# Optimization experiments

Measured on AMD Instinct MI355X. Metric: run time of the kernel, lower is better.

## Reference

```python
import jax, jax.numpy as jnp
import numpy as np

D = 448  # state_dim == input_dim == output_dim

def _param(key, shape):
    # matches torch.rand(shape) * 0.1 + 0.001
    return jax.random.uniform(key, shape, dtype=jnp.float32) * 0.1 + 0.001

def setup_inputs() -> dict:
    key = jax.random.key(0)
    ks = jax.random.split(key, 9)
    x = jax.random.normal(ks[0], (8, 4096, D), dtype=jnp.float32)
    return {
        "x": x,
        "W_q": _param(ks[1], (D, D)),
        "W_k": _param(ks[2], (D, D)),
        "W_v": _param(ks[3], (D, D)),
        "W_o": _param(ks[4], (D, D)),
        "SSM_A": _param(ks[5], (D, D)),
        "SSM_B": _param(ks[6], (D, D)),
        "SSM_C": _param(ks[7], (D, D)),
    }

def reference(x, W_q, W_k, W_v, W_o, SSM_A, SSM_B, SSM_C):
    # seq_len=4096 > threshold=256 -> quadratic SSM path.
    # structured_processing's einsum 'bsd,dd->bsd' multiplies elementwise by
    # the diagonal of the matrix; the block loop is redundant, so we apply the
    # diagonal scale over the whole sequence in one fused op.
    q = jnp.einsum('bsi,id->bsd', x, W_q)
    k = jnp.einsum('bsi,id->bsd', x, W_k)
    v = jnp.einsum('bsi,id->bsd', x, W_v)
    ssm = (q * jnp.diagonal(SSM_A)
           + k * jnp.diagonal(SSM_B)
           + v * jnp.diagonal(SSM_C))
    # dropout is identity in eval mode
    return jnp.einsum('bsd,do->bso', ssm, W_o)
```

## Files before the change

kernel.cpp:

```cpp
#include <hip/hip_runtime.h>
#include <hip/hip_bf16.h>

#define DDIM 448
#define NSTEP 14

typedef __hip_bfloat16 bf16;
typedef __attribute__((ext_vector_type(8))) short short8;
typedef __attribute__((ext_vector_type(4))) float f32x4;

__device__ __forceinline__ short bf_bits(float f) {
    bf16 h = __float2bfloat16(f);
    return *reinterpret_cast<short*>(&h);
}

__device__ __forceinline__ void async16(const bf16* g, bf16* l) {
    __builtin_amdgcn_global_load_lds(
        (const __attribute__((address_space(1))) void*)g,
        (__attribute__((address_space(3))) void*)l, 16, 0, 0);
}

__global__ __launch_bounds__(256) void prep_wc(
    const float* __restrict__ Wq, const float* __restrict__ Wk,
    const float* __restrict__ Wv, const float* __restrict__ Wo,
    const float* __restrict__ Ad, const float* __restrict__ Bd,
    const float* __restrict__ Cd, bf16* __restrict__ Wt)
{
    __shared__ __align__(16) bf16 As[64 * 32];
    __shared__ __align__(16) bf16 Bs[64 * 32];
    __shared__ float da[DDIM], db[DDIM], dc[DDIM];

    const int tid  = threadIdx.x;
    const int i0   = blockIdx.x * 64;
    const int o0   = blockIdx.y * 64;
    const int lane = tid & 63;
    const int wid  = tid >> 6;
    const int wm   = wid >> 1, wn = wid & 1;
    const int m_   = lane & 15, kq = lane >> 4;

    for (int d = tid; d < DDIM; d += 256) {
        da[d] = Ad[d * DDIM + d];
        db[d] = Bd[d * DDIM + d];
        dc[d] = Cd[d * DDIM + d];
    }

    const int dr  = tid >> 3;
    const int oc8 = (tid & 7) * 8;
    const int ir  = tid >> 2;
    const int dc8 = (tid & 3) * 8;

    f32x4 acc[2][2] = {};

    f32x4 w0 = *(const f32x4*)(Wo + dr * DDIM + o0 + oc8);
    f32x4 w1 = *(const f32x4*)(Wo + dr * DDIM + o0 + oc8 + 4);
    f32x4 q0 = *(const f32x4*)(Wq + (i0 + ir) * DDIM + dc8);
    f32x4 q1 = *(const f32x4*)(Wq + (i0 + ir) * DDIM + dc8 + 4);
    f32x4 t0 = *(const f32x4*)(Wk + (i0 + ir) * DDIM + dc8);
    f32x4 t1 = *(const f32x4*)(Wk + (i0 + ir) * DDIM + dc8 + 4);
    f32x4 v0 = *(const f32x4*)(Wv + (i0 + ir) * DDIM + dc8);
    f32x4 v1 = *(const f32x4*)(Wv + (i0 + ir) * DDIM + dc8 + 4);

    for (int k0 = 0; k0 < DDIM; k0 += 32) {
        __syncthreads();
        #pragma unroll
        for (int j = 0; j < 4; ++j) {
            As[(oc8 + j) * 32 + dr]     = __float2bfloat16(w0[j]);
            As[(oc8 + 4 + j) * 32 + dr] = __float2bfloat16(w1[j]);
        }
        short8 e;
        #pragma unroll
        for (int j = 0; j < 4; ++j) {
            e[j]     = bf_bits(q0[j] * da[k0 + dc8 + j]
                             + t0[j] * db[k0 + dc8 + j]
                             + v0[j] * dc[k0 + dc8 + j]);
            e[j + 4] = bf_bits(q1[j] * da[k0 + dc8 + 4 + j]
                             + t1[j] * db[k0 + dc8 + 4 + j]
                             + v1[j] * dc[k0 + dc8 + 4 + j]);
        }
        *(short8*)&Bs[ir * 32 + dc8] = e;
        __syncthreads();

        const int kn = (k0 + 32 < DDIM) ? k0 + 32 : 0;
        w0 = *(const f32x4*)(Wo + (kn + dr) * DDIM + o0 + oc8);
        w1 = *(const f32x4*)(Wo + (kn + dr) * DDIM + o0 + oc8 + 4);
        q0 = *(const f32x4*)(Wq + (i0 + ir) * DDIM + kn + dc8);
        q1 = *(const f32x4*)(Wq + (i0 + ir) * DDIM + kn + dc8 + 4);
        t0 = *(const f32x4*)(Wk + (i0 + ir) * DDIM + kn + dc8);
        t1 = *(const f32x4*)(Wk + (i0 + ir) * DDIM + kn + dc8 + 4);
        v0 = *(const f32x4*)(Wv + (i0 + ir) * DDIM + kn + dc8);
        v1 = *(const f32x4*)(Wv + (i0 + ir) * DDIM + kn + dc8 + 4);

        short8 af[2], bfr[2];
        #pragma unroll
        for (int mi = 0; mi < 2; ++mi)
            af[mi] = *(const short8*)&As[(wm * 32 + mi * 16 + m_) * 32 + kq * 8];
        #pragma unroll
        for (int ni = 0; ni < 2; ++ni)
            bfr[ni] = *(const short8*)&Bs[(wn * 32 + ni * 16 + m_) * 32 + kq * 8];
        #pragma unroll
        for (int mi = 0; mi < 2; ++mi)
            #pragma unroll
            for (int ni = 0; ni < 2; ++ni)
                acc[mi][ni] = __builtin_amdgcn_mfma_f32_16x16x32_bf16(
                    af[mi], bfr[ni], acc[mi][ni], 0, 0, 0);
    }

    #pragma unroll
    for (int mi = 0; mi < 2; ++mi)
        #pragma unroll
        for (int ni = 0; ni < 2; ++ni) {
            const int o = o0 + wm * 32 + mi * 16 + kq * 4;
            const int i = i0 + wn * 32 + ni * 16 + m_;
            bf16* dst = Wt + (i >> 5) * (DDIM * 32) + (i & 31);
            #pragma unroll
            for (int r = 0; r < 4; ++r)
                dst[(o + r) * 32] = __float2bfloat16(acc[mi][ni][r]);
        }
}

__global__ __launch_bounds__(512, 2) void gemm_xwc(
    const float* __restrict__ X, const bf16* __restrict__ Wt,
    float* __restrict__ out)
{
    __shared__ __align__(16) char smem[102400];

    const int tid  = threadIdx.x;
    const int lane = tid & 63;
    const int wid  = tid >> 6;
    const int wr   = wid >> 2;
    const int wc   = wid & 3;
    const int m_   = lane & 15;
    const int kq   = lane >> 4;
    const int row0 = blockIdx.x * 128;

    const int ar = tid >> 2;
    const int ac = (tid & 3) * 8;
    const float* agp = X + (row0 + ar) * DDIM + ac;

    const bf16* bgp = Wt + wc * 7 * 512 + lane * 8;

    f32x4 acc[4][7] = {};

    f32x4 a0 = *(const f32x4*)(agp);
    f32x4 a1 = *(const f32x4*)(agp + 4);
    {
        bf16* A0 = (bf16*)smem;
        short8 w;
        #pragma unroll
        for (int j = 0; j < 4; ++j) {
            w[j] = bf_bits(a0[j]); w[j + 4] = bf_bits(a1[j]);
        }
        *(short8*)&A0[ar * 32 + ac] = w;
    }
    a0 = *(const f32x4*)(agp + 32);
    a1 = *(const f32x4*)(agp + 36);
    if (wid < 4) {
        bf16* B0 = (bf16*)(smem + 16384);
        bf16* B1 = (bf16*)(smem + 16384 + 28672);
        #pragma unroll
        for (int j = 0; j < 7; ++j)
            async16(bgp + j * 512, B0 + (wc * 7 + j) * 512);
        const bf16* b1 = bgp + DDIM * 32;
        #pragma unroll
        for (int j = 0; j < 7; ++j)
            async16(b1 + j * 512, B1 + (wc * 7 + j) * 512);
    }
    asm volatile("s_waitcnt vmcnt(7)" ::: "memory");
    asm volatile("s_waitcnt lgkmcnt(0)" ::: "memory");
    __builtin_amdgcn_s_barrier();

    int bcur = 0;
    int bn2  = 2;
    for (int s = 0; s < NSTEP; ++s) {
        const bf16* Ac = (const bf16*)(smem + ((s & 1) << 13));
        const bf16* Bc = (const bf16*)(smem + 16384 + bcur * 28672);

        if (s + 1 < NSTEP) {
            bf16* An = (bf16*)(smem + (((s + 1) & 1) << 13));
            short8 w;
            #pragma unroll
            for (int j = 0; j < 4; ++j) {
                w[j] = bf_bits(a0[j]); w[j + 4] = bf_bits(a1[j]);
            }
            *(short8*)&An[ar * 32 + ac] = w;
        }
        if (s + 2 < NSTEP) {
            const int k2 = (s + 2) * 32;
            a0 = *(const f32x4*)(agp + k2);
            a1 = *(const f32x4*)(agp + k2 + 4);
        }
        if (s + 2 < NSTEP && wid < 4) {
            bf16* Bn = (bf16*)(smem + 16384 + bn2 * 28672);
            const bf16* bsrc = bgp + (s + 2) * (DDIM * 32);
            #pragma unroll
            for (int j = 0; j < 7; ++j)
                async16(bsrc + j * 512, Bn + (wc * 7 + j) * 512);
        }

        short8 af[4], bfr[7];
        #pragma unroll
        for (int mi = 0; mi < 4; ++mi)
            af[mi] = *(const short8*)&Ac[(wr * 64 + mi * 16 + m_) * 32 + kq * 8];
        #pragma unroll
        for (int ni = 0; ni < 7; ++ni)
            bfr[ni] = *(const short8*)&Bc[(wc * 112 + ni * 16 + m_) * 32 + kq * 8];

        #pragma unroll
        for (int mi = 0; mi < 4; ++mi)
            #pragma unroll
            for (int ni = 0; ni < 7; ++ni)
                acc[mi][ni] = __builtin_amdgcn_mfma_f32_16x16x32_bf16(
                    af[mi], bfr[ni], acc[mi][ni], 0, 0, 0);

        if (s < NSTEP - 2) {
            asm volatile("s_waitcnt vmcnt(9)" ::: "memory");
        } else {
            asm volatile("s_waitcnt vmcnt(0)" ::: "memory");
        }
        asm volatile("s_waitcnt lgkmcnt(0)" ::: "memory");
        __builtin_amdgcn_s_barrier();

        bcur = (bcur == 2) ? 0 : bcur + 1;
        bn2  = (bn2  == 2) ? 0 : bn2  + 1;
    }

    float* Cb = (float*)(smem + 16384);
    #pragma unroll
    for (int t = 0; t < 4; ++t) {
        if (wr == (t >> 1)) {
            #pragma unroll
            for (int mi2 = 0; mi2 < 2; ++mi2) {
                const int mi = (t & 1) * 2 + mi2;
                #pragma unroll
                for (int ni = 0; ni < 7; ++ni) {
                    const int col = wc * 112 + ni * 16 + m_;
                    #pragma unroll
                    for (int r = 0; r < 4; ++r)
                        Cb[(mi2 * 16 + kq * 4 + r) * 452 + col] = acc[mi][ni][r];
                }
            }
        }
        __syncthreads();
        const f32x4* Cb4 = (const f32x4*)Cb;
        f32x4* dst4 = (f32x4*)(out + (row0 + t * 32) * DDIM);
        #pragma unroll
        for (int j = 0; j < 7; ++j) {
            const int v   = j * 512 + tid;
            const int row = v / 112;
            const int cw  = v - row * 112;
            dst4[v] = Cb4[row * 113 + cw];
        }
        __syncthreads();
    }
}

extern "C" void kernel_launch(void* const* d_in, const int* in_sizes, int n_in,
                              void* d_out, int out_size, void* d_ws, size_t ws_size,
                              hipStream_t stream) {
    const float* x  = (const float*)d_in[0];
    const float* Wq = (const float*)d_in[1];
    const float* Wk = (const float*)d_in[2];
    const float* Wv = (const float*)d_in[3];
    const float* Wo = (const float*)d_in[4];
    const float* Ad = (const float*)d_in[5];
    const float* Bd = (const float*)d_in[6];
    const float* Cd = (const float*)d_in[7];

    bf16*  Wt  = (bf16*)d_ws;
    float* out = (float*)d_out;

    const int M = in_sizes[0] / DDIM;

    prep_wc<<<dim3(7, 7), 256, 0, stream>>>(Wq, Wk, Wv, Wo, Ad, Bd, Cd, Wt);
    gemm_xwc<<<M / 128, 512, 0, stream>>>(x, Wt, out);
}
```

Before: 140.1 us.

## Swizzle LDS tiles to avoid bank conflicts and store accumulators directly

Applies an XOR swizzle to the A and B tiles in LDS, covering both the async global-to-LDS writes and the MFMA fragment reads, so the 64-byte-row fragment reads no longer hit conflicting banks. It also drops the LDS-staged epilogue with its barriers and writes accumulator elements straight to global memory. The direct stores are scalar, with 16 lanes per contiguous 64-byte segment, so store coalescing gets worse in exchange for removing the staging and synchronisation.

```diff
diff --git a/kernel.cpp b/kernel.cpp
--- a/kernel.cpp
+++ b/kernel.cpp
@@ -132,24 +132,28 @@
     const int kq   = lane >> 4;
     const int row0 = blockIdx.x * 128;
 
-    const int ar = tid >> 2;
-    const int ac = (tid & 3) * 8;
-    const float* agp = X + (row0 + ar) * DDIM + ac;
-
-    const bf16* bgp = Wt + wc * 7 * 512 + lane * 8;
+    const int ar  = tid >> 2;
+    const int ac4 = tid & 3;
+    const float* agp = X + (row0 + ar) * DDIM + ac4 * 8;
+
+    const int lsw = (lane * 16) ^ (((lane >> 3) & 7) << 4);
+    const bf16* bgp = Wt + wc * 7 * 512 + (lsw >> 1);
+    const int fb  = m_ * 64 + kq * 16;
+    const int fsw = fb ^ (((fb >> 7) & 7) << 4);
+    const int ab  = ar * 64 + ac4 * 16;
+    const int asw = ab ^ (((ab >> 7) & 7) << 4);
 
     f32x4 acc[4][7] = {};
 
     f32x4 a0 = *(const f32x4*)(agp);
     f32x4 a1 = *(const f32x4*)(agp + 4);
     {
-        bf16* A0 = (bf16*)smem;
         short8 w;
         #pragma unroll
         for (int j = 0; j < 4; ++j) {
             w[j] = bf_bits(a0[j]); w[j + 4] = bf_bits(a1[j]);
         }
-        *(short8*)&A0[ar * 32 + ac] = w;
+        *(short8*)(smem + asw) = w;
     }
     a0 = *(const f32x4*)(agp + 32);
     a1 = *(const f32x4*)(agp + 36);
@@ -171,17 +175,17 @@
     int bcur = 0;
     int bn2  = 2;
     for (int s = 0; s < NSTEP; ++s) {
-        const bf16* Ac = (const bf16*)(smem + ((s & 1) << 13));
-        const bf16* Bc = (const bf16*)(smem + 16384 + bcur * 28672);
+        const char* AcB = (const char*)smem + ((s & 1) << 13) + wr * 4096;
+        const char* BcB = (const char*)smem + 16384 + bcur * 28672 + wc * 7168;
 
         if (s + 1 < NSTEP) {
-            bf16* An = (bf16*)(smem + (((s + 1) & 1) << 13));
+            char* An = (char*)smem + (((s + 1) & 1) << 13);
             short8 w;
             #pragma unroll
             for (int j = 0; j < 4; ++j) {
                 w[j] = bf_bits(a0[j]); w[j + 4] = bf_bits(a1[j]);
             }
-            *(short8*)&An[ar * 32 + ac] = w;
+            *(short8*)(An + asw) = w;
         }
         if (s + 2 < NSTEP) {
             const int k2 = (s + 2) * 32;
@@ -199,10 +203,10 @@
         short8 af[4], bfr[7];
         #pragma unroll
         for (int mi = 0; mi < 4; ++mi)
-            af[mi] = *(const short8*)&Ac[(wr * 64 + mi * 16 + m_) * 32 + kq * 8];
+            af[mi] = *(const short8*)(AcB + mi * 1024 + fsw);
         #pragma unroll
         for (int ni = 0; ni < 7; ++ni)
-            bfr[ni] = *(const short8*)&Bc[(wc * 112 + ni * 16 + m_) * 32 + kq * 8];
+            bfr[ni] = *(const short8*)(BcB + ni * 1024 + fsw);
 
         #pragma unroll
         for (int mi = 0; mi < 4; ++mi)
@@ -223,33 +227,18 @@
         bn2  = (bn2  == 2) ? 0 : bn2  + 1;
     }
 
-    float* Cb = (float*)(smem + 16384);
-    #pragma unroll
-    for (int t = 0; t < 4; ++t) {
-        if (wr == (t >> 1)) {
-            #pragma unroll
-            for (int mi2 = 0; mi2 < 2; ++mi2) {
-                const int mi = (t & 1) * 2 + mi2;
+    {
+        const int crow = row0 + wr * 64 + kq * 4;
+        const int ccol = wc * 112 + m_;
+        #pragma unroll
+        for (int mi = 0; mi < 4; ++mi)
+            #pragma unroll
+            for (int ni = 0; ni < 7; ++ni) {
+                float* dst = out + (crow + mi * 16) * DDIM + ccol + ni * 16;
                 #pragma unroll
-                for (int ni = 0; ni < 7; ++ni) {
-                    const int col = wc * 112 + ni * 16 + m_;
-                    #pragma unroll
-                    for (int r = 0; r < 4; ++r)
-                        Cb[(mi2 * 16 + kq * 4 + r) * 452 + col] = acc[mi][ni][r];
-                }
+                for (int r = 0; r < 4; ++r)
+                    dst[r * DDIM] = acc[mi][ni][r];
             }
-        }
-        __syncthreads();
-        const f32x4* Cb4 = (const f32x4*)Cb;
-        f32x4* dst4 = (f32x4*)(out + (row0 + t * 32) * DDIM);
-        #pragma unroll
-        for (int j = 0; j < 7; ++j) {
-            const int v   = j * 512 + tid;
-            const int row = v / 112;
-            const int cw  = v - row * 112;
-            dst4[v] = Cb4[row * 113 + cw];
-        }
-        __syncthreads();
     }
 }
 
```

Result: no change. 140.1 us (-0.0%).
